# Optimization experiments

Measured on AMD Instinct MI355X. Metric: run time of the kernel, lower is better.

The kernel has to match this reference:

```python
import jax, jax.numpy as jnp
import numpy as np

HIDDEN = 32
FEAT = 30
POS = 2

def setup_inputs() -> dict:
    key = jax.random.key(0)
    ks = jax.random.split(key, 12)
    B, T = 4096, 512
    x = jax.random.normal(ks[0], (B, T, FEAT), dtype=jnp.float32)
    # last feature is the OBJECT_IN_SCENE_BIT: 0/1 flag
    bit = (jax.random.uniform(ks[1], (B, T)) > 0.3).astype(jnp.float32)
    x = x.at[..., -1].set(bit)
    h0 = jax.random.normal(ks[2], (1, B, HIDDEN), dtype=jnp.float32)
    c0 = jax.random.normal(ks[3], (1, B, HIDDEN), dtype=jnp.float32)
    s_ih = 1.0 / np.sqrt(HIDDEN)
    W_ih = jax.random.uniform(ks[4], (4 * HIDDEN, FEAT), minval=-s_ih, maxval=s_ih)
    W_hh = jax.random.uniform(ks[5], (4 * HIDDEN, HIDDEN), minval=-s_ih, maxval=s_ih)
    b_ih = jax.random.uniform(ks[6], (4 * HIDDEN,), minval=-s_ih, maxval=s_ih)
    b_hh = jax.random.uniform(ks[7], (4 * HIDDEN,), minval=-s_ih, maxval=s_ih)
    W_all = jax.random.uniform(ks[8], (HIDDEN, HIDDEN), minval=-s_ih, maxval=s_ih)
    b_all = jnp.zeros((HIDDEN,), jnp.float32)
    W_pos = jax.random.uniform(ks[9], (POS, HIDDEN), minval=-s_ih, maxval=s_ih)
    b_pos = jnp.zeros((POS,), jnp.float32)
    W_lv = jax.random.uniform(ks[10], (1, HIDDEN), minval=-s_ih, maxval=s_ih)
    b_lv = jnp.zeros((1,), jnp.float32)
    return {"x": x, "h0": h0, "c0": c0, "W_ih": W_ih, "W_hh": W_hh,
            "b_ih": b_ih, "b_hh": b_hh, "W_all": W_all, "b_all": b_all,
            "W_pos": W_pos, "b_pos": b_pos, "W_lv": W_lv, "b_lv": b_lv}

def _masked_lstm_scan(x, h0, c0, W_ih, W_hh, b_ih, b_hh):
    # x: [B,T,F]; h0,c0: [B,H]. Mask = last feature == 1.
    def step(carry, x_t):
        h, c = carry                      # [B,H]
        gates = x_t @ W_ih.T + b_ih + h @ W_hh.T + b_hh  # [B,4H]
        i, f, g, o = jnp.split(gates, 4, axis=-1)
        i, f, o = jax.nn.sigmoid(i), jax.nn.sigmoid(f), jax.nn.sigmoid(o)
        g = jnp.tanh(g)
        c_new = f * c + i * g
        h_new = o * jnp.tanh(c_new)
        m = (x_t[:, -1:] == 1.0)          # [B,1] object-in-scene mask
        h2 = jnp.where(m, h_new, h)
        c2 = jnp.where(m, c_new, c)
        out = jnp.where(m, h_new, 0.0)    # invalid_output = zeros
        return (h2, c2), out
    (hT, cT), hs = jax.lax.scan(step, (h0, c0), jnp.swapaxes(x, 0, 1))
    return jnp.swapaxes(hs, 0, 1), hT, cT  # hs: [B,T,H]

def reference(x, h0, c0, W_ih, W_hh, b_ih, b_hh, W_all, b_all, W_pos, b_pos, W_lv, b_lv):
    hs, hT, cT = _masked_lstm_scan(x, h0[0], c0[0], W_ih, W_hh, b_ih, b_hh)
    fc_hidden = hs @ W_all.T + b_all                 # all_fc (dropout is eval-mode identity)
    position_pred = fc_hidden @ W_pos.T + b_pos      # [B,T,2]
    leave_scene_pred = jax.nn.sigmoid(hs @ W_lv.T + b_lv)  # [B,T,1]
    return position_pred, leave_scene_pred, hT[None], cT[None]
```

## Files before the change

### kernel.cpp

```cpp
#include <hip/hip_runtime.h>
#include <stdint.h>

#define T_STEPS 512
#define F_IN 30
#define HID 32
#define LOG2E 1.44269504088896340736f

typedef __attribute__((ext_vector_type(8))) short short8;
typedef __attribute__((ext_vector_type(4))) float floatx4;

#define MFMA(a, b, c) __builtin_amdgcn_mfma_f32_16x16x32_bf16((a), (b), (c), 0, 0, 0)

__device__ __forceinline__ unsigned short f2bf(float f) {
    uint32_t u = __float_as_uint(f);
    u += 0x7fffu + ((u >> 16) & 1u);
    return (unsigned short)(u >> 16);
}
__device__ __forceinline__ float bf2f(unsigned short h) {
    return __uint_as_float(((uint32_t)h) << 16);
}
__device__ __forceinline__ uint32_t cvtpk(float a, float b) {
    uint32_t r;
    asm("v_cvt_pk_bf16_f32 %0, %1, %2" : "=v"(r) : "v"(a), "v"(b));
    return r;
}
__device__ __forceinline__ float rcp_f(float x) { return __builtin_amdgcn_rcpf(x); }
#if __has_builtin(__builtin_amdgcn_exp2f)
__device__ __forceinline__ float exp2_f(float x) { return __builtin_amdgcn_exp2f(x); }
#else
__device__ __forceinline__ float exp2_f(float x) { return exp2f(x); }
#endif

__device__ __forceinline__ void loadx8(float (&d)[8], const float* p, bool tail) {
    float2 a0 = *(const float2*)(p + 0);
    float2 a1 = *(const float2*)(p + 2);
    float2 a2 = *(const float2*)(p + 4);
    float2 a3 = make_float2(0.f, 0.f);
    if (!tail) a3 = *(const float2*)(p + 6);
    d[0]=a0.x; d[1]=a0.y; d[2]=a1.x; d[3]=a1.y;
    d[4]=a2.x; d[5]=a2.y; d[6]=a3.x; d[7]=a3.y;
}

__global__ __launch_bounds__(64, 1)
void lstm_wave_kernel(const float* __restrict__ x, const float* __restrict__ h0,
                      const float* __restrict__ c0, const float* __restrict__ W_ih,
                      const float* __restrict__ W_hh, const float* __restrict__ b_ih,
                      const float* __restrict__ b_hh, const float* __restrict__ W_all,
                      const float* __restrict__ b_all, const float* __restrict__ W_pos,
                      const float* __restrict__ b_pos, const float* __restrict__ W_lv,
                      const float* __restrict__ b_lv, float* __restrict__ pos_out,
                      float* __restrict__ lv_out, float* __restrict__ hT_out,
                      float* __restrict__ cT_out)
{
    const int lane = threadIdx.x;
    const int quad = lane >> 4;
    const int l15  = lane & 15;
    const int row  = blockIdx.x * 16 + l15;

    short8 wxh[8], wxl[8], whh[8], whl[8];
#pragma unroll
    for (int mt = 0; mt < 8; ++mt) {
        const float gs = ((mt == 4) || (mt == 5) ? -2.0f : -1.0f) * LOG2E;
        const int m = mt * 16 + l15;
        const int c = m & 31;
        const int u = 8 * ((c & 15) >> 2) + 4 * (c >> 4) + (c & 3);
        const int R = (m >> 5) * 32 + u;
        const float bias = (b_ih[R] + b_hh[R]) * gs;
#pragma unroll
        for (int j = 0; j < 8; ++j) {
            const int k = quad * 8 + j;
            float wx = (k < F_IN) ? W_ih[R * F_IN + k] * gs : (k == F_IN ? bias : 0.0f);
            unsigned short hx = f2bf(wx);
            wxh[mt][j] = (short)hx; wxl[mt][j] = (short)f2bf(wx - bf2f(hx));
            float wh = W_hh[R * HID + k] * gs;
            unsigned short hh = f2bf(wh);
            whh[mt][j] = (short)hh; whl[mt][j] = (short)f2bf(wh - bf2f(hh));
        }
    }

    short8 wph, wpl;
#pragma unroll
    for (int j = 0; j < 8; ++j) {
        const int k = quad * 8 + j;
        float w = 0.0f;
        if (l15 == 0)      { for (int o = 0; o < HID; ++o) w += W_pos[o]       * W_all[o * HID + k]; }
        else if (l15 == 1) { for (int o = 0; o < HID; ++o) w += W_pos[HID + o] * W_all[o * HID + k]; }
        else if (l15 == 2) { w = W_lv[k]; }
        unsigned short hw_ = f2bf(w);
        wph[j] = (short)hw_; wpl[j] = (short)f2bf(w - bf2f(hw_));
    }
    float bc0 = b_pos[0], bc1 = b_pos[1];
    for (int o = 0; o < HID; ++o) { bc0 += W_pos[o] * b_all[o]; bc1 += W_pos[HID + o] * b_all[o]; }
    const float blv = b_lv[0];

    union HU { uint32_t u[4]; short8 s; };
    float cst[8];
    HU Hh, Hl;
    {
        const float* hp = h0 + (size_t)row * HID + quad * 8;
        const float* cp = c0 + (size_t)row * HID + quad * 8;
        float hv[8];
#pragma unroll
        for (int j = 0; j < 8; ++j) { hv[j] = hp[j]; cst[j] = cp[j]; }
#pragma unroll
        for (int w = 0; w < 4; ++w) {
            const uint32_t ph = cvtpk(hv[2 * w], hv[2 * w + 1]);
            const float r0 = hv[2 * w]     - __uint_as_float(ph << 16);
            const float r1 = hv[2 * w + 1] - __uint_as_float(ph & 0xffff0000u);
            Hh.u[w] = ph; Hl.u[w] = cvtpk(r0, r1);
        }
    }

    const float* xlane = x + (size_t)row * T_STEPS * F_IN + quad * 8;
    const float* mptr  = x + (size_t)row * T_STEPS * F_IN + (F_IN - 1);
    const bool tail = (quad == 3);

    float xr0[8] = {0,0,0,0,0,0,0,0}, xr1[8] = {0,0,0,0,0,0,0,0};
    float xr2[8] = {0,0,0,0,0,0,0,0}, xr3[8] = {0,0,0,0,0,0,0,0};
    float mr0, mr1, mr2, mr3;
    loadx8(xr0, xlane + 0 * F_IN, tail);  mr0 = mptr[0 * F_IN];
    loadx8(xr1, xlane + 1 * F_IN, tail);  mr1 = mptr[1 * F_IN];
    loadx8(xr2, xlane + 2 * F_IN, tail);  mr2 = mptr[2 * F_IN];
    loadx8(xr3, xlane + 3 * F_IN, tail);  mr3 = mptr[3 * F_IN];

    auto step = [&](int t, float (&xr)[8], float& mr) {
        const float mcur = mr;
        HU xu;
        xu.u[0] = cvtpk(xr[0], xr[1]);
        xu.u[1] = cvtpk(xr[2], xr[3]);
        xu.u[2] = cvtpk(xr[4], xr[5]);
        xu.u[3] = tail ? 0x3f803f80u : cvtpk(xr[6], xr[7]);
        const short8 xah = xu.s;
        const short8 hah = Hh.s, hal = Hl.s;
        {
            const int tp = (t + 4 < T_STEPS) ? t + 4 : (T_STEPS - 1);
            loadx8(xr, xlane + (size_t)tp * F_IN, tail);
            mr = mptr[(size_t)tp * F_IN];
        }
        floatx4 acc[8];
#pragma unroll
        for (int mt = 0; mt < 8; ++mt) {
            floatx4 a = {0.f, 0.f, 0.f, 0.f};
            a = MFMA(wxh[mt], xah, a);
            a = MFMA(wxl[mt], xah, a);
            a = MFMA(whh[mt], hah, a);
            a = MFMA(whh[mt], hal, a);
            a = MFMA(whl[mt], hah, a);
            acc[mt] = a;
        }
        float act[8][4];
#pragma unroll
        for (int mt = 0; mt < 8; ++mt) {
            const bool isg = (mt == 4) || (mt == 5);
#pragma unroll
            for (int r = 0; r < 4; ++r) {
                const float rr = rcp_f(1.0f + exp2_f(acc[mt][r]));
                act[mt][r] = isg ? fmaf(2.0f, rr, -1.0f) : rr;
            }
        }
        const bool on = (mcur == 1.0f);
        float hn[8];
#pragma unroll
        for (int j = 0; j < 8; ++j) {
            const int tI = j >> 2, r = j & 3;
            const float gi = act[0 + tI][r], gf = act[2 + tI][r];
            const float gg = act[4 + tI][r], go = act[6 + tI][r];
            const float cn = gf * cst[j] + gi * gg;
            const float tn = fmaf(2.0f, rcp_f(1.0f + exp2_f(-2.0f * LOG2E * cn)), -1.0f);
            hn[j] = go * tn;
            cst[j] = on ? cn : cst[j];
        }
        HU Oh, Ol;
#pragma unroll
        for (int w = 0; w < 4; ++w) {
            const uint32_t ph = cvtpk(hn[2 * w], hn[2 * w + 1]);
            const float r0 = hn[2 * w]     - __uint_as_float(ph << 16);
            const float r1 = hn[2 * w + 1] - __uint_as_float(ph & 0xffff0000u);
            const uint32_t pl = cvtpk(r0, r1);
            Oh.u[w] = on ? ph : 0u;
            Ol.u[w] = on ? pl : 0u;
            Hh.u[w] = on ? ph : Hh.u[w];
            Hl.u[w] = on ? pl : Hl.u[w];
        }
        floatx4 ha = {0.f, 0.f, 0.f, 0.f};
        ha = MFMA(wph, Oh.s, ha);
        ha = MFMA(wph, Ol.s, ha);
        ha = MFMA(wpl, Oh.s, ha);
        if (quad == 0) {
            const size_t o = (size_t)row * T_STEPS + t;
            *(float2*)&pos_out[o * 2] = make_float2(ha[0] + bc0, ha[1] + bc1);
            const float z = ha[2] + blv;
            lv_out[o] = rcp_f(1.0f + exp2_f(-LOG2E * z));
        }
    };

#pragma unroll 1
    for (int t = 0; t < T_STEPS; t += 4) {
        step(t + 0, xr0, mr0);
        step(t + 1, xr1, mr1);
        step(t + 2, xr2, mr2);
        step(t + 3, xr3, mr3);
    }

    {
        float* hp = hT_out + (size_t)row * HID + quad * 8;
        float* cp = cT_out + (size_t)row * HID + quad * 8;
#pragma unroll
        for (int w = 0; w < 4; ++w) {
            hp[2 * w]     = __uint_as_float(Hh.u[w] << 16)        + __uint_as_float(Hl.u[w] << 16);
            hp[2 * w + 1] = __uint_as_float(Hh.u[w] & 0xffff0000u) + __uint_as_float(Hl.u[w] & 0xffff0000u);
        }
#pragma unroll
        for (int j = 0; j < 8; ++j) cp[j] = cst[j];
    }
}

extern "C" void kernel_launch(void* const* d_in, const int* in_sizes, int n_in,
                              void* d_out, int out_size, void* d_ws, size_t ws_size,
                              hipStream_t stream) {
    const float* x     = (const float*)d_in[0];
    const float* h0    = (const float*)d_in[1];
    const float* c0    = (const float*)d_in[2];
    const float* W_ih  = (const float*)d_in[3];
    const float* W_hh  = (const float*)d_in[4];
    const float* b_ih  = (const float*)d_in[5];
    const float* b_hh  = (const float*)d_in[6];
    const float* W_all = (const float*)d_in[7];
    const float* b_all = (const float*)d_in[8];
    const float* W_pos = (const float*)d_in[9];
    const float* b_pos = (const float*)d_in[10];
    const float* W_lv  = (const float*)d_in[11];
    const float* b_lv  = (const float*)d_in[12];

    const int B = in_sizes[1] / HID;
    float* out     = (float*)d_out;
    float* pos_out = out;
    float* lv_out  = pos_out + (size_t)B * T_STEPS * 2;
    float* hT_out  = lv_out  + (size_t)B * T_STEPS;
    float* cT_out  = hT_out  + (size_t)B * HID;

    dim3 grid(B / 16), block(64);
    hipLaunchKernelGGL(lstm_wave_kernel, grid, block, 0, stream,
                       x, h0, c0, W_ih, W_hh, b_ih, b_hh, W_all, b_all,
                       W_pos, b_pos, W_lv, b_lv, pos_out, lv_out, hT_out, cT_out);
}
```

Before: 733.6 us.

## Software-pipeline input projection and output head off the recurrent critical path

Computes the x·W_ih MFMA contribution for step t+1 during step t, and defers the position/leave-scene head for step t-1 into step t. Only the h·W_hh MFMAs and activations stay on the serial dependency chain, so the independent MFMAs can overlap with it. The cost is more live registers (eight extra accumulator vectors plus the carried Oh/Ol) and an epilogue for the last timestep. The prefetch reload of the current x buffer is moved after the next-step conversion so the buffer is not overwritten too early.

```diff
diff --git a/kernel.cpp b/kernel.cpp
--- a/kernel.cpp
+++ b/kernel.cpp
@@ -123,30 +123,66 @@
     loadx8(xr2, xlane + 2 * F_IN, tail);  mr2 = mptr[2 * F_IN];
     loadx8(xr3, xlane + 3 * F_IN, tail);  mr3 = mptr[3 * F_IN];
 
-    auto step = [&](int t, float (&xr)[8], float& mr) {
-        const float mcur = mr;
+    floatx4 accx_p[8];
+    {
         HU xu;
-        xu.u[0] = cvtpk(xr[0], xr[1]);
-        xu.u[1] = cvtpk(xr[2], xr[3]);
-        xu.u[2] = cvtpk(xr[4], xr[5]);
-        xu.u[3] = tail ? 0x3f803f80u : cvtpk(xr[6], xr[7]);
-        const short8 xah = xu.s;
+        xu.u[0] = cvtpk(xr0[0], xr0[1]);
+        xu.u[1] = cvtpk(xr0[2], xr0[3]);
+        xu.u[2] = cvtpk(xr0[4], xr0[5]);
+        xu.u[3] = tail ? 0x3f803f80u : cvtpk(xr0[6], xr0[7]);
+#pragma unroll
+        for (int mt = 0; mt < 8; ++mt) {
+            floatx4 a = {0.f, 0.f, 0.f, 0.f};
+            a = MFMA(wxh[mt], xu.s, a);
+            a = MFMA(wxl[mt], xu.s, a);
+            accx_p[mt] = a;
+        }
+    }
+    HU Oh, Ol;
+#pragma unroll
+    for (int w = 0; w < 4; ++w) { Oh.u[w] = 0u; Ol.u[w] = 0u; }
+
+    auto step = [&](int t, float (&xr_cur)[8], float& mr_cur, float (&xr_nxt)[8]) {
+        const float mcur = mr_cur;
         const short8 hah = Hh.s, hal = Hl.s;
-        {
-            const int tp = (t + 4 < T_STEPS) ? t + 4 : (T_STEPS - 1);
-            loadx8(xr, xlane + (size_t)tp * F_IN, tail);
-            mr = mptr[(size_t)tp * F_IN];
-        }
         floatx4 acc[8];
 #pragma unroll
         for (int mt = 0; mt < 8; ++mt) {
-            floatx4 a = {0.f, 0.f, 0.f, 0.f};
-            a = MFMA(wxh[mt], xah, a);
-            a = MFMA(wxl[mt], xah, a);
+            floatx4 a = accx_p[mt];
             a = MFMA(whh[mt], hah, a);
             a = MFMA(whh[mt], hal, a);
             a = MFMA(whl[mt], hah, a);
             acc[mt] = a;
+        }
+        HU xu;
+        xu.u[0] = cvtpk(xr_nxt[0], xr_nxt[1]);
+        xu.u[1] = cvtpk(xr_nxt[2], xr_nxt[3]);
+        xu.u[2] = cvtpk(xr_nxt[4], xr_nxt[5]);
+        xu.u[3] = tail ? 0x3f803f80u : cvtpk(xr_nxt[6], xr_nxt[7]);
+        floatx4 accx_n[8];
+#pragma unroll
+        for (int mt = 0; mt < 8; ++mt) {
+            floatx4 a = {0.f, 0.f, 0.f, 0.f};
+            a = MFMA(wxh[mt], xu.s, a);
+            a = MFMA(wxl[mt], xu.s, a);
+            accx_n[mt] = a;
+        }
+        if (t != 0) {
+            floatx4 ha = {0.f, 0.f, 0.f, 0.f};
+            ha = MFMA(wph, Oh.s, ha);
+            ha = MFMA(wph, Ol.s, ha);
+            ha = MFMA(wpl, Oh.s, ha);
+            if (quad == 0) {
+                const size_t o = (size_t)row * T_STEPS + (t - 1);
+                *(float2*)&pos_out[o * 2] = make_float2(ha[0] + bc0, ha[1] + bc1);
+                const float z = ha[2] + blv;
+                lv_out[o] = rcp_f(1.0f + exp2_f(-LOG2E * z));
+            }
+        }
+        {
+            const int tp = (t + 4 < T_STEPS) ? t + 4 : (T_STEPS - 1);
+            loadx8(xr_cur, xlane + (size_t)tp * F_IN, tail);
+            mr_cur = mptr[(size_t)tp * F_IN];
         }
         float act[8][4];
 #pragma unroll
@@ -170,7 +206,6 @@
             hn[j] = go * tn;
             cst[j] = on ? cn : cst[j];
         }
-        HU Oh, Ol;
 #pragma unroll
         for (int w = 0; w < 4; ++w) {
             const uint32_t ph = cvtpk(hn[2 * w], hn[2 * w + 1]);
@@ -182,24 +217,29 @@
             Hh.u[w] = on ? ph : Hh.u[w];
             Hl.u[w] = on ? pl : Hl.u[w];
         }
+#pragma unroll
+        for (int mt = 0; mt < 8; ++mt) accx_p[mt] = accx_n[mt];
+    };
+
+#pragma unroll 1
+    for (int t = 0; t < T_STEPS; t += 4) {
+        step(t + 0, xr0, mr0, xr1);
+        step(t + 1, xr1, mr1, xr2);
+        step(t + 2, xr2, mr2, xr3);
+        step(t + 3, xr3, mr3, xr0);
+    }
+
+    {
         floatx4 ha = {0.f, 0.f, 0.f, 0.f};
         ha = MFMA(wph, Oh.s, ha);
         ha = MFMA(wph, Ol.s, ha);
         ha = MFMA(wpl, Oh.s, ha);
         if (quad == 0) {
-            const size_t o = (size_t)row * T_STEPS + t;
+            const size_t o = (size_t)row * T_STEPS + (T_STEPS - 1);
             *(float2*)&pos_out[o * 2] = make_float2(ha[0] + bc0, ha[1] + bc1);
             const float z = ha[2] + blv;
             lv_out[o] = rcp_f(1.0f + exp2_f(-LOG2E * z));
         }
-    };
-
-#pragma unroll 1
-    for (int t = 0; t < T_STEPS; t += 4) {
-        step(t + 0, xr0, mr0);
-        step(t + 1, xr1, mr1);
-        step(t + 2, xr2, mr2);
-        step(t + 3, xr3, mr3);
     }
 
     {
```

New measurement: 789.0 us. +7.6%, slower.

## Split LSTM gate computation across four waves with LDS exchange per step

Applied to the files above, without the earlier changes.

Each 16-row block now runs four wavefronts, each computing two of the eight gate tiles, then exchanging activations through shared memory with barriers every step. The output projection is deferred by one step and handled by wave 3 so it overlaps with the next step's gate MFMAs. This shortens the per-step serial MFMA and transcendental chain per wave, at the cost of two block barriers and LDS round-trips per timestep. With 256 blocks of 256 threads, parallelism per CU increases from one wave.

```diff
diff --git a/kernel.cpp b/kernel.cpp
--- a/kernel.cpp
+++ b/kernel.cpp
@@ -10,6 +10,8 @@
 typedef __attribute__((ext_vector_type(4))) float floatx4;
 
 #define MFMA(a, b, c) __builtin_amdgcn_mfma_f32_16x16x32_bf16((a), (b), (c), 0, 0, 0)
+
+#define BAR() asm volatile("s_waitcnt lgkmcnt(0)\n\ts_barrier" ::: "memory")
 
 __device__ __forceinline__ unsigned short f2bf(float f) {
     uint32_t u = __float_as_uint(f);
@@ -41,8 +43,8 @@
     d[4]=a2.x; d[5]=a2.y; d[6]=a3.x; d[7]=a3.y;
 }
 
-__global__ __launch_bounds__(64, 1)
-void lstm_wave_kernel(const float* __restrict__ x, const float* __restrict__ h0,
+__global__ __launch_bounds__(256, 1)
+void lstm_quad_kernel(const float* __restrict__ x, const float* __restrict__ h0,
                       const float* __restrict__ c0, const float* __restrict__ W_ih,
                       const float* __restrict__ W_hh, const float* __restrict__ b_ih,
                       const float* __restrict__ b_hh, const float* __restrict__ W_all,
@@ -52,16 +54,25 @@
                       float* __restrict__ lv_out, float* __restrict__ hT_out,
                       float* __restrict__ cT_out)
 {
-    const int lane = threadIdx.x;
+    const int tid  = threadIdx.x;
+    const int wv   = tid >> 6;
+    const int lane = tid & 63;
     const int quad = lane >> 4;
     const int l15  = lane & 15;
     const int row  = blockIdx.x * 16 + l15;
 
-    short8 wxh[8], wxl[8], whh[8], whl[8];
+    __shared__ float gbuf[16][132];
+    __shared__ __align__(16) unsigned short hbh[16][40];
+    __shared__ __align__(16) unsigned short hbl[16][40];
+    __shared__ __align__(16) unsigned short obh[16][40];
+    __shared__ __align__(16) unsigned short obl[16][40];
+
+    const bool  isg = (wv == 2);
+    const float gs  = (isg ? -2.0f : -1.0f) * LOG2E;
+    short8 wxh[2], wxl[2], whh[2], whl[2];
 #pragma unroll
-    for (int mt = 0; mt < 8; ++mt) {
-        const float gs = ((mt == 4) || (mt == 5) ? -2.0f : -1.0f) * LOG2E;
-        const int m = mt * 16 + l15;
+    for (int s = 0; s < 2; ++s) {
+        const int m = (2 * wv + s) * 16 + l15;
         const int c = m & 31;
         const int u = 8 * ((c & 15) >> 2) + 4 * (c >> 4) + (c & 3);
         const int R = (m >> 5) * 32 + u;
@@ -71,10 +82,10 @@
             const int k = quad * 8 + j;
             float wx = (k < F_IN) ? W_ih[R * F_IN + k] * gs : (k == F_IN ? bias : 0.0f);
             unsigned short hx = f2bf(wx);
-            wxh[mt][j] = (short)hx; wxl[mt][j] = (short)f2bf(wx - bf2f(hx));
+            wxh[s][j] = (short)hx; wxl[s][j] = (short)f2bf(wx - bf2f(hx));
             float wh = W_hh[R * HID + k] * gs;
             unsigned short hh = f2bf(wh);
-            whh[mt][j] = (short)hh; whl[mt][j] = (short)f2bf(wh - bf2f(hh));
+            whh[s][j] = (short)hh; whl[s][j] = (short)f2bf(wh - bf2f(hh));
         }
     }
 
@@ -93,105 +104,113 @@
     for (int o = 0; o < HID; ++o) { bc0 += W_pos[o] * b_all[o]; bc1 += W_pos[HID + o] * b_all[o]; }
     const float blv = b_lv[0];
 
-    union HU { uint32_t u[4]; short8 s; };
-    float cst[8];
-    HU Hh, Hl;
+    const int u0 = 8 * quad + 2 * wv;
+    float c_st0, c_st1, h_st0, h_st1;
     {
-        const float* hp = h0 + (size_t)row * HID + quad * 8;
-        const float* cp = c0 + (size_t)row * HID + quad * 8;
-        float hv[8];
-#pragma unroll
-        for (int j = 0; j < 8; ++j) { hv[j] = hp[j]; cst[j] = cp[j]; }
-#pragma unroll
-        for (int w = 0; w < 4; ++w) {
-            const uint32_t ph = cvtpk(hv[2 * w], hv[2 * w + 1]);
-            const float r0 = hv[2 * w]     - __uint_as_float(ph << 16);
-            const float r1 = hv[2 * w + 1] - __uint_as_float(ph & 0xffff0000u);
-            Hh.u[w] = ph; Hl.u[w] = cvtpk(r0, r1);
-        }
+        const float2 cc = *(const float2*)&c0[(size_t)row * HID + u0];
+        const float2 hh2 = *(const float2*)&h0[(size_t)row * HID + u0];
+        c_st0 = cc.x; c_st1 = cc.y; h_st0 = hh2.x; h_st1 = hh2.y;
+        const uint32_t ph = cvtpk(h_st0, h_st1);
+        const float r0 = h_st0 - __uint_as_float(ph << 16);
+        const float r1 = h_st1 - __uint_as_float(ph & 0xffff0000u);
+        *(uint32_t*)&hbh[l15][u0] = ph;
+        *(uint32_t*)&hbl[l15][u0] = cvtpk(r0, r1);
+        *(uint32_t*)&obh[l15][u0] = 0u;
+        *(uint32_t*)&obl[l15][u0] = 0u;
     }
 
     const float* xlane = x + (size_t)row * T_STEPS * F_IN + quad * 8;
     const float* mptr  = x + (size_t)row * T_STEPS * F_IN + (F_IN - 1);
     const bool tail = (quad == 3);
 
-    float xr0[8] = {0,0,0,0,0,0,0,0}, xr1[8] = {0,0,0,0,0,0,0,0};
-    float xr2[8] = {0,0,0,0,0,0,0,0}, xr3[8] = {0,0,0,0,0,0,0,0};
+    float xr0[8], xr1[8], xr2[8], xr3[8];
     float mr0, mr1, mr2, mr3;
     loadx8(xr0, xlane + 0 * F_IN, tail);  mr0 = mptr[0 * F_IN];
     loadx8(xr1, xlane + 1 * F_IN, tail);  mr1 = mptr[1 * F_IN];
     loadx8(xr2, xlane + 2 * F_IN, tail);  mr2 = mptr[2 * F_IN];
     loadx8(xr3, xlane + 3 * F_IN, tail);  mr3 = mptr[3 * F_IN];
 
+    BAR();
+
+    union HU { uint32_t u[4]; short8 s; };
+
     auto step = [&](int t, float (&xr)[8], float& mr) {
         const float mcur = mr;
+        const short8 hah = *(const short8*)&hbh[l15][quad * 8];
+        const short8 hal = *(const short8*)&hbl[l15][quad * 8];
+        short8 oah, oal;
+        if (wv == 3 && t > 0) {
+            oah = *(const short8*)&obh[l15][quad * 8];
+            oal = *(const short8*)&obl[l15][quad * 8];
+        }
         HU xu;
         xu.u[0] = cvtpk(xr[0], xr[1]);
         xu.u[1] = cvtpk(xr[2], xr[3]);
         xu.u[2] = cvtpk(xr[4], xr[5]);
         xu.u[3] = tail ? 0x3f803f80u : cvtpk(xr[6], xr[7]);
-        const short8 xah = xu.s;
-        const short8 hah = Hh.s, hal = Hl.s;
         {
             const int tp = (t + 4 < T_STEPS) ? t + 4 : (T_STEPS - 1);
             loadx8(xr, xlane + (size_t)tp * F_IN, tail);
             mr = mptr[(size_t)tp * F_IN];
         }
-        floatx4 acc[8];
-#pragma unroll
-        for (int mt = 0; mt < 8; ++mt) {
-            floatx4 a = {0.f, 0.f, 0.f, 0.f};
-            a = MFMA(wxh[mt], xah, a);
-            a = MFMA(wxl[mt], xah, a);
-            a = MFMA(whh[mt], hah, a);
-            a = MFMA(whh[mt], hal, a);
-            a = MFMA(whl[mt], hah, a);
-            acc[mt] = a;
-        }
-        float act[8][4];
-#pragma unroll
-        for (int mt = 0; mt < 8; ++mt) {
-            const bool isg = (mt == 4) || (mt == 5);
-#pragma unroll
-            for (int r = 0; r < 4; ++r) {
-                const float rr = rcp_f(1.0f + exp2_f(acc[mt][r]));
-                act[mt][r] = isg ? fmaf(2.0f, rr, -1.0f) : rr;
+        floatx4 a0 = {0.f, 0.f, 0.f, 0.f}, a1 = {0.f, 0.f, 0.f, 0.f};
+        a0 = MFMA(wxh[0], xu.s, a0);  a1 = MFMA(wxh[1], xu.s, a1);
+        a0 = MFMA(wxl[0], xu.s, a0);  a1 = MFMA(wxl[1], xu.s, a1);
+        a0 = MFMA(whh[0], hah, a0);   a1 = MFMA(whh[1], hah, a1);
+        a0 = MFMA(whh[0], hal, a0);   a1 = MFMA(whh[1], hal, a1);
+        a0 = MFMA(whl[0], hah, a0);   a1 = MFMA(whl[1], hah, a1);
+        if (wv == 3 && t > 0) {
+            floatx4 ha = {0.f, 0.f, 0.f, 0.f};
+            ha = MFMA(wph, oah, ha);
+            ha = MFMA(wph, oal, ha);
+            ha = MFMA(wpl, oah, ha);
+            if (quad == 0) {
+                const size_t o = (size_t)row * T_STEPS + (t - 1);
+                *(float2*)&pos_out[o * 2] = make_float2(ha[0] + bc0, ha[1] + bc1);
+                lv_out[o] = rcp_f(1.0f + exp2_f(-LOG2E * (ha[2] + blv)));
             }
         }
+        float4 v0, v1;
+        {
+            const float q00 = rcp_f(1.0f + exp2_f(a0[0])), q01 = rcp_f(1.0f + exp2_f(a0[1]));
+            const float q02 = rcp_f(1.0f + exp2_f(a0[2])), q03 = rcp_f(1.0f + exp2_f(a0[3]));
+            const float q10 = rcp_f(1.0f + exp2_f(a1[0])), q11 = rcp_f(1.0f + exp2_f(a1[1]));
+            const float q12 = rcp_f(1.0f + exp2_f(a1[2])), q13 = rcp_f(1.0f + exp2_f(a1[3]));
+            if (isg) {
+                v0 = make_float4(fmaf(2.f,q00,-1.f), fmaf(2.f,q01,-1.f), fmaf(2.f,q02,-1.f), fmaf(2.f,q03,-1.f));
+                v1 = make_float4(fmaf(2.f,q10,-1.f), fmaf(2.f,q11,-1.f), fmaf(2.f,q12,-1.f), fmaf(2.f,q13,-1.f));
+            } else {
+                v0 = make_float4(q00, q01, q02, q03);
+                v1 = make_float4(q10, q11, q12, q13);
+            }
+        }
+        *(float4*)&gbuf[l15][32 * wv + 4 * quad]      = v0;
+        *(float4*)&gbuf[l15][32 * wv + 16 + 4 * quad] = v1;
+        BAR();
+        const int goff = 16 * (wv >> 1) + 4 * quad + 2 * (wv & 1);
+        const float2 gi = *(const float2*)&gbuf[l15][goff];
+        const float2 gf = *(const float2*)&gbuf[l15][32 + goff];
+        const float2 gg = *(const float2*)&gbuf[l15][64 + goff];
+        const float2 go = *(const float2*)&gbuf[l15][96 + goff];
         const bool on = (mcur == 1.0f);
-        float hn[8];
-#pragma unroll
-        for (int j = 0; j < 8; ++j) {
-            const int tI = j >> 2, r = j & 3;
-            const float gi = act[0 + tI][r], gf = act[2 + tI][r];
-            const float gg = act[4 + tI][r], go = act[6 + tI][r];
-            const float cn = gf * cst[j] + gi * gg;
-            const float tn = fmaf(2.0f, rcp_f(1.0f + exp2_f(-2.0f * LOG2E * cn)), -1.0f);
-            hn[j] = go * tn;
-            cst[j] = on ? cn : cst[j];
-        }
-        HU Oh, Ol;
-#pragma unroll
-        for (int w = 0; w < 4; ++w) {
-            const uint32_t ph = cvtpk(hn[2 * w], hn[2 * w + 1]);
-            const float r0 = hn[2 * w]     - __uint_as_float(ph << 16);
-            const float r1 = hn[2 * w + 1] - __uint_as_float(ph & 0xffff0000u);
-            const uint32_t pl = cvtpk(r0, r1);
-            Oh.u[w] = on ? ph : 0u;
-            Ol.u[w] = on ? pl : 0u;
-            Hh.u[w] = on ? ph : Hh.u[w];
-            Hl.u[w] = on ? pl : Hl.u[w];
-        }
-        floatx4 ha = {0.f, 0.f, 0.f, 0.f};
-        ha = MFMA(wph, Oh.s, ha);
-        ha = MFMA(wph, Ol.s, ha);
-        ha = MFMA(wpl, Oh.s, ha);
-        if (quad == 0) {
-            const size_t o = (size_t)row * T_STEPS + t;
-            *(float2*)&pos_out[o * 2] = make_float2(ha[0] + bc0, ha[1] + bc1);
-            const float z = ha[2] + blv;
-            lv_out[o] = rcp_f(1.0f + exp2_f(-LOG2E * z));
-        }
+        const float cn0 = gf.x * c_st0 + gi.x * gg.x;
+        const float tn0 = fmaf(2.0f, rcp_f(1.0f + exp2_f(-2.0f * LOG2E * cn0)), -1.0f);
+        const float hn0 = go.x * tn0;
+        const float cn1 = gf.y * c_st1 + gi.y * gg.y;
+        const float tn1 = fmaf(2.0f, rcp_f(1.0f + exp2_f(-2.0f * LOG2E * cn1)), -1.0f);
+        const float hn1 = go.y * tn1;
+        if (on) { c_st0 = cn0; c_st1 = cn1; h_st0 = hn0; h_st1 = hn1; }
+        const uint32_t ph = cvtpk(hn0, hn1);
+        const float r0 = hn0 - __uint_as_float(ph << 16);
+        const float r1 = hn1 - __uint_as_float(ph & 0xffff0000u);
+        const uint32_t pl = cvtpk(r0, r1);
+        *(uint32_t*)&obh[l15][u0] = on ? ph : 0u;
+        *(uint32_t*)&obl[l15][u0] = on ? pl : 0u;
+        if (on) {
+            *(uint32_t*)&hbh[l15][u0] = ph;
+            *(uint32_t*)&hbl[l15][u0] = pl;
+        }
+        BAR();
     };
 
 #pragma unroll 1
@@ -202,17 +221,22 @@
         step(t + 3, xr3, mr3);
     }
 
-    {
-        float* hp = hT_out + (size_t)row * HID + quad * 8;
-        float* cp = cT_out + (size_t)row * HID + quad * 8;
-#pragma unroll
-        for (int w = 0; w < 4; ++w) {
-            hp[2 * w]     = __uint_as_float(Hh.u[w] << 16)        + __uint_as_float(Hl.u[w] << 16);
-            hp[2 * w + 1] = __uint_as_float(Hh.u[w] & 0xffff0000u) + __uint_as_float(Hl.u[w] & 0xffff0000u);
-        }
-#pragma unroll
-        for (int j = 0; j < 8; ++j) cp[j] = cst[j];
-    }
+    if (wv == 3) {
+        const short8 oah = *(const short8*)&obh[l15][quad * 8];
+        const short8 oal = *(const short8*)&obl[l15][quad * 8];
+        floatx4 ha = {0.f, 0.f, 0.f, 0.f};
+        ha = MFMA(wph, oah, ha);
+        ha = MFMA(wph, oal, ha);
+        ha = MFMA(wpl, oah, ha);
+        if (quad == 0) {
+            const size_t o = (size_t)row * T_STEPS + (T_STEPS - 1);
+            *(float2*)&pos_out[o * 2] = make_float2(ha[0] + bc0, ha[1] + bc1);
+            lv_out[o] = rcp_f(1.0f + exp2_f(-LOG2E * (ha[2] + blv)));
+        }
+    }
+
+    *(float2*)&hT_out[(size_t)row * HID + u0] = make_float2(h_st0, h_st1);
+    *(float2*)&cT_out[(size_t)row * HID + u0] = make_float2(c_st0, c_st1);
 }
 
 extern "C" void kernel_launch(void* const* d_in, const int* in_sizes, int n_in,
@@ -239,8 +263,8 @@
     float* hT_out  = lv_out  + (size_t)B * T_STEPS;
     float* cT_out  = hT_out  + (size_t)B * HID;
 
-    dim3 grid(B / 16), block(64);
-    hipLaunchKernelGGL(lstm_wave_kernel, grid, block, 0, stream,
+    dim3 grid(B / 16), block(256);
+    hipLaunchKernelGGL(lstm_quad_kernel, grid, block, 0, stream,
                        x, h0, c0, W_ih, W_hh, b_ih, b_hh, W_all, b_all,
                        W_pos, b_pos, W_lv, b_lv, pos_out, lv_out, hT_out, cT_out);
 }
```

Result: faster. 638.6 us (-12.9%).
